# Optimization experiments

Measured on AMD Instinct MI355X. Metric: run time of the kernel, lower is better.

Reference implementation:

```python
import jax, jax.numpy as jnp
import numpy as np

B, S, D, E, K = 8, 4096, 2048, 64, 8


def setup_inputs() -> dict:
    key = jax.random.key(0)
    ks = jax.random.split(key, 4)
    x = jax.random.normal(ks[0], (B, S, D), dtype=jnp.float32)
    noise = jax.random.normal(ks[1], (B, S, E), dtype=jnp.float32)
    scale = 1.0 / np.sqrt(D)
    W_linear = jax.random.normal(ks[2], (E, D), dtype=jnp.float32) * scale
    W_noise = jax.random.normal(ks[3], (E, D), dtype=jnp.float32) * scale
    b_linear = jnp.zeros((E,), dtype=jnp.float32)
    b_noise = jnp.zeros((E,), dtype=jnp.float32)
    return {"x": x, "noise": noise, "W_linear": W_linear, "b_linear": b_linear,
            "W_noise": W_noise, "b_noise": b_noise}


def reference(x, noise, W_linear, b_linear, W_noise, b_noise):
    # logits / noise_logits: [B,S,E]
    logits = jnp.einsum('bsd,ed->bse', x, W_linear) + b_linear
    noise_logits = jnp.einsum('bsd,ed->bse', x, W_noise) + b_noise
    noisy = logits + noise * jax.nn.softplus(noise_logits)
    topk_vals, indices = jax.lax.top_k(noisy, K)  # [B,S,K]
    # scatter top-k values into a -inf tensor, softmax over experts
    flat_vals = topk_vals.reshape(-1, K)
    flat_idx = indices.reshape(-1, K)
    N = flat_idx.shape[0]
    sparse = jnp.full((N, E), -jnp.inf, dtype=noisy.dtype)
    sparse = sparse.at[jnp.arange(N)[:, None], flat_idx].set(flat_vals)
    router_output = jax.nn.softmax(sparse, axis=-1).reshape(B, S, E)
    return router_output, indices
```

## Files before the change

### kernel.cpp

```cpp
#include <hip/hip_runtime.h>
#include <hip/hip_bf16.h>
#include <math.h>

namespace {
constexpr int DD = 2048;
constexpr int EE = 64;
constexpr int KK = 8;
constexpr int TPB = 64;
constexpr int MS = 128;
constexpr int NMEGA = DD / MS;
constexpr int NTH = 256;
constexpr int XB = TPB * MS * 4;
constexpr float TAU = 2e-4f;
}

typedef __attribute__((ext_vector_type(8))) short short8;
typedef __attribute__((ext_vector_type(4))) float f32x4;

#define RES(t, e) res[(t) * 129 + (e)]

__device__ inline void split_bf16(float v, ushort& h, ushort& l) {
    __hip_bfloat16 hb = __float2bfloat16(v);
    float hf = __bfloat162float(hb);
    __hip_bfloat16 lb = __float2bfloat16(v - hf);
    h = __builtin_bit_cast(ushort, hb);
    l = __builtin_bit_cast(ushort, lb);
}

__device__ inline void conv_tile(const float4& A, const float4& B, short8& hi, short8& lo) {
    const float f[8] = {A.x, A.y, A.z, A.w, B.x, B.y, B.z, B.w};
#pragma unroll
    for (int i = 0; i < 8; ++i) {
        ushort h, l;
        split_bf16(f[i], h, l);
        hi[i] = (short)h;
        lo[i] = (short)l;
    }
}

__device__ inline void gload_lds16(const void* g, void* l) {
    __builtin_amdgcn_global_load_lds(
        (const __attribute__((address_space(1))) unsigned int*)g,
        (__attribute__((address_space(3))) unsigned int*)l,
        16, 0, 0);
}

#define STAGE(m_, c_)                                                                  \
    do {                                                                               \
        unsigned char* xb_ = smem + (c_) * XB;                                         \
        _Pragma("unroll")                                                              \
        for (int j = 0; j < 8; ++j) {                                                  \
            const int row_ = (w * 8 + j) * 2 + (lane >> 5);                            \
            const int u_   = lane & 31;                                                \
            const float* g_ = x + (tok0 + row_) * (long)DD + (long)(m_) * MS           \
                              + ((u_ ^ (row_ & 7)) << 2);                              \
            gload_lds16(g_, xb_ + (w * 8 + j) * 1024);                                 \
        }                                                                              \
    } while (0)

#define LOADW(dst_, m_, ss_)                                                           \
    do {                                                                               \
        _Pragma("unroll")                                                              \
        for (int el_ = 0; el_ < 4; ++el_) {                                            \
            const size_t b_ = ((size_t)(((m_) * 4 + (ss_)) * 8 + eq * 4 + el_)) * 128; \
            dst_[el_ * 2]     = wp[b_];                                                \
            dst_[el_ * 2 + 1] = wp[b_ + 64];                                           \
        }                                                                              \
    } while (0)

__global__ __launch_bounds__(256)
void prep_w(const float* __restrict__ Wl, const float* __restrict__ Wn,
            ushort* __restrict__ wsB)
{
    const int t    = blockIdx.x * 256 + threadIdx.x;
    const int lane = t & 63;
    const int et   = (t >> 6) & 7;
    const int s    = t >> 9;
    const int e    = et * 16 + (lane & 15);
    const int k    = s * 32 + ((lane >> 4) * 8);
    const float* src = (e < EE) ? &Wl[(long)e * DD + k] : &Wn[(long)(e - EE) * DD + k];
    const float4 f0 = *reinterpret_cast<const float4*>(src);
    const float4 f1 = *reinterpret_cast<const float4*>(src + 4);
    const float f[8] = {f0.x, f0.y, f0.z, f0.w, f1.x, f1.y, f1.z, f1.w};
    uint hw[4], lw[4];
#pragma unroll
    for (int j = 0; j < 4; ++j) {
        ushort h0, l0, h1, l1;
        split_bf16(f[2 * j], h0, l0);
        split_bf16(f[2 * j + 1], h1, l1);
        hw[j] = (uint)h0 | ((uint)h1 << 16);
        lw[j] = (uint)l0 | ((uint)l1 << 16);
    }
    const size_t chunk = ((size_t)(s * 8 + et)) * 1024;
    *reinterpret_cast<uint4*>(&wsB[chunk + lane * 8])       = make_uint4(hw[0], hw[1], hw[2], hw[3]);
    *reinterpret_cast<uint4*>(&wsB[chunk + 512 + lane * 8]) = make_uint4(lw[0], lw[1], lw[2], lw[3]);
}

__global__ __launch_bounds__(NTH, 2)
void router_main(const float* __restrict__ x,
                 const float* __restrict__ noise,
                 const ushort* __restrict__ wsB,
                 const float* __restrict__ Wl, const float* __restrict__ bl,
                 const float* __restrict__ Wn, const float* __restrict__ bn,
                 float* __restrict__ out_router, float* __restrict__ out_idx)
{
    __shared__ __align__(16) unsigned char smem[2 * XB];
    __shared__ float  tkv[TPB][KK];
    __shared__ int    tki[TPB][KK];
    __shared__ int    cand[TPB][10];
    __shared__ int    amb_list[TPB];
    __shared__ int    amb_count;
    __shared__ double dsh[20];

    const int tid  = threadIdx.x;
    const int lane = tid & 63;
    const int w    = tid >> 6;
    const int mh   = w >> 1;
    const int eq   = w & 1;
    const long tok0 = (long)blockIdx.x * TPB;
    if (tid == 0) amb_count = 0;

    const uint4* wp = reinterpret_cast<const uint4*>(wsB) + lane;

    f32x4 acc[2][4];
#pragma unroll
    for (int mt = 0; mt < 2; ++mt)
#pragma unroll
        for (int e = 0; e < 4; ++e) acc[mt][e] = {0.f, 0.f, 0.f, 0.f};

    uint4 W0[8], W1[8], W2[8], W3[8];
    STAGE(0, 0);
    LOADW(W0, 0, 0);
    LOADW(W1, 0, 1);
    __syncthreads();

    const int colr = lane & 15;
    const int krow = lane >> 4;

    for (int m = 0; m < NMEGA; ++m) {
        const int cur = m & 1;
        if (m + 1 < NMEGA) STAGE(m + 1, cur ^ 1);
        const unsigned char* xb = smem + cur * XB;
#pragma unroll
        for (int ss = 0; ss < 4; ++ss) {
            if (ss == 0)      LOADW(W2, m, 2);
            else if (ss == 1) LOADW(W3, m, 3);
            else if (ss == 2) { if (m + 1 < NMEGA) LOADW(W0, m + 1, 0); }
            else              { if (m + 1 < NMEGA) LOADW(W1, m + 1, 1); }

            short8 ah[2], al[2];
#pragma unroll
            for (int mt = 0; mt < 2; ++mt) {
                const int r = mh * 32 + mt * 16 + colr;
                const unsigned char* base = xb + r * 512;
                const int v0 = ss * 8 + krow * 2;
                const float4 f0 = *reinterpret_cast<const float4*>(base + ((v0 ^ (r & 7)) << 4));
                const float4 f1 = *reinterpret_cast<const float4*>(base + (((v0 + 1) ^ (r & 7)) << 4));
                conv_tile(f0, f1, ah[mt], al[mt]);
            }
            const uint4* Wc = (ss == 0) ? W0 : (ss == 1) ? W1 : (ss == 2) ? W2 : W3;
#pragma unroll
            for (int el = 0; el < 4; ++el) {
                const short8 bh  = __builtin_bit_cast(short8, Wc[el * 2]);
                const short8 bl2 = __builtin_bit_cast(short8, Wc[el * 2 + 1]);
                acc[0][el] = __builtin_amdgcn_mfma_f32_16x16x32_bf16(ah[0], bh,  acc[0][el], 0, 0, 0);
                acc[1][el] = __builtin_amdgcn_mfma_f32_16x16x32_bf16(ah[1], bh,  acc[1][el], 0, 0, 0);
                acc[0][el] = __builtin_amdgcn_mfma_f32_16x16x32_bf16(al[0], bh,  acc[0][el], 0, 0, 0);
                acc[1][el] = __builtin_amdgcn_mfma_f32_16x16x32_bf16(al[1], bh,  acc[1][el], 0, 0, 0);
                acc[0][el] = __builtin_amdgcn_mfma_f32_16x16x32_bf16(ah[0], bl2, acc[0][el], 0, 0, 0);
                acc[1][el] = __builtin_amdgcn_mfma_f32_16x16x32_bf16(ah[1], bl2, acc[1][el], 0, 0, 0);
            }
        }
        __syncthreads();
    }

    float* res = reinterpret_cast<float*>(smem);
    {
        const int rg = (lane >> 4) * 4;
#pragma unroll
        for (int mt = 0; mt < 2; ++mt)
#pragma unroll
            for (int el = 0; el < 4; ++el) {
                const int e = (eq * 4 + el) * 16 + colr;
                const float bias = (e < EE) ? bl[e] : bn[e - EE];
#pragma unroll
                for (int r = 0; r < 4; ++r)
                    RES(mh * 32 + mt * 16 + rg + r, e) = acc[mt][el][r] + bias;
            }
    }
    __syncthreads();

    {
        const int t  = tid >> 2;
        const int e0 = (tid & 3) * 16;
        const float* nrow = &noise[(tok0 + t) * (long)EE];
#pragma unroll 4
        for (int j = 0; j < 16; ++j) {
            const int e = e0 + j;
            const float z  = RES(t, EE + e);
            const float sp = fmaxf(z, 0.f) + log1pf(expf(-fabsf(z)));
            RES(t, e) = RES(t, e) + nrow[e] * sp;
        }
    }
    __syncthreads();

    {
        const int t   = tid >> 2;
        const int sub = tid & 3;
        float lv[10]; int li[10];
#pragma unroll
        for (int k = 0; k < 10; ++k) {
            float best = -INFINITY;
            int bi = sub * 16;
#pragma unroll
            for (int j = 0; j < 16; ++j) {
                const int e = sub * 16 + j;
                const float v = RES(t, e);
                if (v > best) { best = v; bi = e; }
            }
#pragma unroll
            for (int m = 1; m < 4; m <<= 1) {
                const float ov = __shfl_xor(best, m, 64);
                const int   oi = __shfl_xor(bi, m, 64);
                if (ov > best || (ov == best && oi < bi)) { best = ov; bi = oi; }
            }
            lv[k] = best; li[k] = bi;
            if ((bi >> 4) == sub) RES(t, bi) = -INFINITY;
        }
        bool amb = false;
#pragma unroll
        for (int k = 0; k < 9; ++k) amb |= (lv[k] - lv[k + 1] < TAU);
        const float mmax = lv[0];
        float p[KK];
        float sm = 0.f;
#pragma unroll
        for (int k = 0; k < KK; ++k) { p[k] = expf(lv[k] - mmax); sm += p[k]; }
        const float inv = 1.f / sm;
        if (sub == 0) {
#pragma unroll
            for (int k = 0; k < KK; ++k) { tkv[t][k] = p[k] * inv; tki[t][k] = li[k]; }
            if (amb) {
                const int pos = atomicAdd(&amb_count, 1);
                amb_list[pos] = t;
#pragma unroll
                for (int c = 0; c < 10; ++c) cand[t][c] = li[c];
            }
        }
    }
    __syncthreads();

    const int namb = amb_count;
    for (int a = 0; a < namb; ++a) {
        const int t = amb_list[a];
        {
            const float4* xsrc = reinterpret_cast<const float4*>(&x[(tok0 + t) * (long)DD]);
            float4* xd = reinterpret_cast<float4*>(smem);
            xd[tid * 2]     = xsrc[tid * 2];
            xd[tid * 2 + 1] = xsrc[tid * 2 + 1];
        }
        __syncthreads();
        {
            const int g  = tid >> 3;
            const int gs = tid & 7;
            double dsum = 0.0;
            if (g < 20) {
                const int c = (g < 10) ? g : g - 10;
                const int e = cand[t][c];
                const float* wr = (g < 10) ? &Wl[(long)e * DD] : &Wn[(long)e * DD];
                const float* xs = reinterpret_cast<const float*>(smem);
                for (int k = gs * 4; k < DD; k += 32) {
                    const float4 xv = *reinterpret_cast<const float4*>(&xs[k]);
                    const float4 wv = *reinterpret_cast<const float4*>(&wr[k]);
                    dsum = fma((double)xv.x, (double)wv.x, dsum);
                    dsum = fma((double)xv.y, (double)wv.y, dsum);
                    dsum = fma((double)xv.z, (double)wv.z, dsum);
                    dsum = fma((double)xv.w, (double)wv.w, dsum);
                }
            }
#pragma unroll
            for (int m = 1; m < 8; m <<= 1) dsum += __shfl_xor(dsum, m, 64);
            if (g < 20 && (tid & 7) == 0) dsh[g] = dsum;
        }
        __syncthreads();
        if (tid < 64) {
            double val; int idx;
            if (tid < 10) {
                const int e = cand[t][tid];
                const double v  = dsh[tid] + (double)bl[e];
                const double z  = dsh[10 + tid] + (double)bn[e];
                const double sp = fmax(z, 0.0) + log1p(exp(-fabs(z)));
                val = v + (double)noise[(tok0 + t) * (long)EE + e] * sp;
                idx = e;
            } else { val = -INFINITY; idx = 64 + tid; }
            double sel[KK]; int sidx[KK];
#pragma unroll
            for (int k = 0; k < KK; ++k) {
                double mv = val; int mi = idx;
#pragma unroll
                for (int m = 1; m < 64; m <<= 1) {
                    const double ov = __shfl_xor(mv, m, 64);
                    const int   oi = __shfl_xor(mi, m, 64);
                    if (ov > mv || (ov == mv && oi < mi)) { mv = ov; mi = oi; }
                }
                sel[k] = mv; sidx[k] = mi;
                if (idx == mi) val = -INFINITY;
            }
            if (tid == 0) {
                const double mx = sel[0];
                double p[KK]; double sm = 0.0;
#pragma unroll
                for (int k = 0; k < KK; ++k) { p[k] = exp(sel[k] - mx); sm += p[k]; }
                const double inv = 1.0 / sm;
#pragma unroll
                for (int k = 0; k < KK; ++k) {
                    tkv[t][k] = (float)(p[k] * inv);
                    tki[t][k] = sidx[k];
                }
            }
        }
        __syncthreads();
    }

    {
        const int t  = tid >> 2;
        const int e0 = (tid & 3) * 16;
        int   ki[KK];
        float kv[KK];
#pragma unroll
        for (int k = 0; k < KK; ++k) { ki[k] = tki[t][k]; kv[k] = tkv[t][k]; }
        float4 v[4];
        float* vf = reinterpret_cast<float*>(v);
#pragma unroll
        for (int j = 0; j < 16; ++j) {
            float val = 0.f;
#pragma unroll
            for (int k = 0; k < KK; ++k)
                val = (ki[k] == e0 + j) ? kv[k] : val;
            vf[j] = val;
        }
        float4* dst = reinterpret_cast<float4*>(&out_router[(tok0 + t) * (long)EE + e0]);
#pragma unroll
        for (int q = 0; q < 4; ++q) dst[q] = v[q];
    }
    {
        const int f = tid * 2;
        const int t = f >> 3;
        const int k0i = f & 7;
        out_idx[(tok0 + t) * (long)KK + k0i]     = (float)tki[t][k0i];
        out_idx[(tok0 + t) * (long)KK + k0i + 1] = (float)tki[t][k0i + 1];
    }
}

extern "C" void kernel_launch(void* const* d_in, const int* in_sizes, int n_in,
                              void* d_out, int out_size, void* d_ws, size_t ws_size,
                              hipStream_t stream) {
    const float* x     = (const float*)d_in[0];
    const float* noise = (const float*)d_in[1];
    const float* Wl    = (const float*)d_in[2];
    const float* bl    = (const float*)d_in[3];
    const float* Wn    = (const float*)d_in[4];
    const float* bn    = (const float*)d_in[5];

    const int M = in_sizes[0] / DD;
    float* out_router = (float*)d_out;
    float* out_idx    = (float*)d_out + (long)M * EE;
    ushort* wsB = (ushort*)d_ws;

    hipLaunchKernelGGL(prep_w, dim3(128), dim3(256), 0, stream, Wl, Wn, wsB);
    hipLaunchKernelGGL(router_main, dim3(M / TPB), dim3(NTH), 0, stream,
                       x, noise, wsB, Wl, bl, Wn, bn, out_router, out_idx);
}
```

Before: 160.6 us.

## Double block to 512 threads, each wave computing one 16-token tile

The main router kernel now uses 8 waves per block instead of 4. Each wave handles a single 16-row M tile instead of two, which halves the accumulator and A-fragment registers, and launch bounds now request 4 blocks per CU. The staging, softplus/noise, and output-write phases are redistributed over 512 threads, and the top-k and ambiguity phases are gated to the first 256 threads. This raises parallelism and latency hiding but loses the reuse of each loaded B (weight) fragment across two M tiles, so per-wave weight register traffic doubles relative to MFMA work.

```diff
diff --git a/kernel.cpp b/kernel.cpp
--- a/kernel.cpp
+++ b/kernel.cpp
@@ -9,7 +9,7 @@
 constexpr int TPB = 64;
 constexpr int MS = 128;
 constexpr int NMEGA = DD / MS;
-constexpr int NTH = 256;
+constexpr int NTH = 512;
 constexpr int XB = TPB * MS * 4;
 constexpr float TAU = 2e-4f;
 }
@@ -49,12 +49,13 @@
     do {                                                                               \
         unsigned char* xb_ = smem + (c_) * XB;                                         \
         _Pragma("unroll")                                                              \
-        for (int j = 0; j < 8; ++j) {                                                  \
-            const int row_ = (w * 8 + j) * 2 + (lane >> 5);                            \
+        for (int j = 0; j < 4; ++j) {                                                  \
+            const int ch_  = w * 4 + j;                                                \
+            const int row_ = ch_ * 2 + (lane >> 5);                                    \
             const int u_   = lane & 31;                                                \
             const float* g_ = x + (tok0 + row_) * (long)DD + (long)(m_) * MS           \
                               + ((u_ ^ (row_ & 7)) << 2);                              \
-            gload_lds16(g_, xb_ + (w * 8 + j) * 1024);                                 \
+            gload_lds16(g_, xb_ + ch_ * 1024);                                         \
         }                                                                              \
     } while (0)
 
@@ -96,7 +97,7 @@
     *reinterpret_cast<uint4*>(&wsB[chunk + 512 + lane * 8]) = make_uint4(lw[0], lw[1], lw[2], lw[3]);
 }
 
-__global__ __launch_bounds__(NTH, 2)
+__global__ __launch_bounds__(NTH, 4)
 void router_main(const float* __restrict__ x,
                  const float* __restrict__ noise,
                  const ushort* __restrict__ wsB,
@@ -115,18 +116,16 @@
     const int tid  = threadIdx.x;
     const int lane = tid & 63;
     const int w    = tid >> 6;
-    const int mh   = w >> 1;
+    const int tg   = w >> 1;
     const int eq   = w & 1;
     const long tok0 = (long)blockIdx.x * TPB;
     if (tid == 0) amb_count = 0;
 
     const uint4* wp = reinterpret_cast<const uint4*>(wsB) + lane;
 
-    f32x4 acc[2][4];
-#pragma unroll
-    for (int mt = 0; mt < 2; ++mt)
-#pragma unroll
-        for (int e = 0; e < 4; ++e) acc[mt][e] = {0.f, 0.f, 0.f, 0.f};
+    f32x4 acc[4];
+#pragma unroll
+    for (int e = 0; e < 4; ++e) acc[e] = {0.f, 0.f, 0.f, 0.f};
 
     uint4 W0[8], W1[8], W2[8], W3[8];
     STAGE(0, 0);
@@ -148,27 +147,23 @@
             else if (ss == 2) { if (m + 1 < NMEGA) LOADW(W0, m + 1, 0); }
             else              { if (m + 1 < NMEGA) LOADW(W1, m + 1, 1); }
 
-            short8 ah[2], al[2];
-#pragma unroll
-            for (int mt = 0; mt < 2; ++mt) {
-                const int r = mh * 32 + mt * 16 + colr;
+            short8 ah, al;
+            {
+                const int r = tg * 16 + colr;
                 const unsigned char* base = xb + r * 512;
                 const int v0 = ss * 8 + krow * 2;
                 const float4 f0 = *reinterpret_cast<const float4*>(base + ((v0 ^ (r & 7)) << 4));
                 const float4 f1 = *reinterpret_cast<const float4*>(base + (((v0 + 1) ^ (r & 7)) << 4));
-                conv_tile(f0, f1, ah[mt], al[mt]);
+                conv_tile(f0, f1, ah, al);
             }
             const uint4* Wc = (ss == 0) ? W0 : (ss == 1) ? W1 : (ss == 2) ? W2 : W3;
 #pragma unroll
             for (int el = 0; el < 4; ++el) {
                 const short8 bh  = __builtin_bit_cast(short8, Wc[el * 2]);
                 const short8 bl2 = __builtin_bit_cast(short8, Wc[el * 2 + 1]);
-                acc[0][el] = __builtin_amdgcn_mfma_f32_16x16x32_bf16(ah[0], bh,  acc[0][el], 0, 0, 0);
-                acc[1][el] = __builtin_amdgcn_mfma_f32_16x16x32_bf16(ah[1], bh,  acc[1][el], 0, 0, 0);
-                acc[0][el] = __builtin_amdgcn_mfma_f32_16x16x32_bf16(al[0], bh,  acc[0][el], 0, 0, 0);
-                acc[1][el] = __builtin_amdgcn_mfma_f32_16x16x32_bf16(al[1], bh,  acc[1][el], 0, 0, 0);
-                acc[0][el] = __builtin_amdgcn_mfma_f32_16x16x32_bf16(ah[0], bl2, acc[0][el], 0, 0, 0);
-                acc[1][el] = __builtin_amdgcn_mfma_f32_16x16x32_bf16(ah[1], bl2, acc[1][el], 0, 0, 0);
+                acc[el] = __builtin_amdgcn_mfma_f32_16x16x32_bf16(ah, bh,  acc[el], 0, 0, 0);
+                acc[el] = __builtin_amdgcn_mfma_f32_16x16x32_bf16(al, bh,  acc[el], 0, 0, 0);
+                acc[el] = __builtin_amdgcn_mfma_f32_16x16x32_bf16(ah, bl2, acc[el], 0, 0, 0);
             }
         }
         __syncthreads();
@@ -178,33 +173,33 @@
     {
         const int rg = (lane >> 4) * 4;
 #pragma unroll
-        for (int mt = 0; mt < 2; ++mt)
-#pragma unroll
-            for (int el = 0; el < 4; ++el) {
-                const int e = (eq * 4 + el) * 16 + colr;
-                const float bias = (e < EE) ? bl[e] : bn[e - EE];
-#pragma unroll
-                for (int r = 0; r < 4; ++r)
-                    RES(mh * 32 + mt * 16 + rg + r, e) = acc[mt][el][r] + bias;
-            }
+        for (int el = 0; el < 4; ++el) {
+            const int e = (eq * 4 + el) * 16 + colr;
+            const float bias = (e < EE) ? bl[e] : bn[e - EE];
+#pragma unroll
+            for (int r = 0; r < 4; ++r)
+                RES(tg * 16 + rg + r, e) = acc[el][r] + bias;
+        }
     }
     __syncthreads();
 
     {
-        const int t  = tid >> 2;
-        const int e0 = (tid & 3) * 16;
-        const float* nrow = &noise[(tok0 + t) * (long)EE];
-#pragma unroll 4
-        for (int j = 0; j < 16; ++j) {
+        const int t  = tid >> 3;
+        const int e0 = (tid & 7) * 8;
+        const float4 n0 = *reinterpret_cast<const float4*>(&noise[(tok0 + t) * (long)EE + e0]);
+        const float4 n1 = *reinterpret_cast<const float4*>(&noise[(tok0 + t) * (long)EE + e0 + 4]);
+        const float nv[8] = {n0.x, n0.y, n0.z, n0.w, n1.x, n1.y, n1.z, n1.w};
+#pragma unroll
+        for (int j = 0; j < 8; ++j) {
             const int e = e0 + j;
             const float z  = RES(t, EE + e);
             const float sp = fmaxf(z, 0.f) + log1pf(expf(-fabsf(z)));
-            RES(t, e) = RES(t, e) + nrow[e] * sp;
+            RES(t, e) = RES(t, e) + nv[j] * sp;
         }
     }
     __syncthreads();
 
-    {
+    if (tid < 256) {
         const int t   = tid >> 2;
         const int sub = tid & 3;
         float lv[10]; int li[10];
@@ -252,7 +247,7 @@
     const int namb = amb_count;
     for (int a = 0; a < namb; ++a) {
         const int t = amb_list[a];
-        {
+        if (tid < 256) {
             const float4* xsrc = reinterpret_cast<const float4*>(&x[(tok0 + t) * (long)DD]);
             float4* xd = reinterpret_cast<float4*>(smem);
             xd[tid * 2]     = xsrc[tid * 2];
@@ -322,32 +317,29 @@
     }
 
     {
-        const int t  = tid >> 2;
-        const int e0 = (tid & 3) * 16;
+        const int t  = tid >> 3;
+        const int e0 = (tid & 7) * 8;
         int   ki[KK];
         float kv[KK];
 #pragma unroll
         for (int k = 0; k < KK; ++k) { ki[k] = tki[t][k]; kv[k] = tkv[t][k]; }
-        float4 v[4];
-        float* vf = reinterpret_cast<float*>(v);
-#pragma unroll
-        for (int j = 0; j < 16; ++j) {
+        float v[8];
+#pragma unroll
+        for (int j = 0; j < 8; ++j) {
             float val = 0.f;
 #pragma unroll
             for (int k = 0; k < KK; ++k)
                 val = (ki[k] == e0 + j) ? kv[k] : val;
-            vf[j] = val;
-        }
-        float4* dst = reinterpret_cast<float4*>(&out_router[(tok0 + t) * (long)EE + e0]);
-#pragma unroll
-        for (int q = 0; q < 4; ++q) dst[q] = v[q];
+            v[j] = val;
+        }
+        float* dst = &out_router[(tok0 + t) * (long)EE + e0];
+        *reinterpret_cast<float4*>(dst)     = make_float4(v[0], v[1], v[2], v[3]);
+        *reinterpret_cast<float4*>(dst + 4) = make_float4(v[4], v[5], v[6], v[7]);
     }
     {
-        const int f = tid * 2;
-        const int t = f >> 3;
-        const int k0i = f & 7;
-        out_idx[(tok0 + t) * (long)KK + k0i]     = (float)tki[t][k0i];
-        out_idx[(tok0 + t) * (long)KK + k0i + 1] = (float)tki[t][k0i + 1];
+        const int t = tid >> 3;
+        const int k = tid & 7;
+        out_idx[(tok0 + t) * (long)KK + k] = (float)tki[t][k];
     }
 }
 
```

New measurement: 185.0 us. 1.15x slower.

## Halve x mega-tile and W register buffers to run four blocks per CU

Applied to the files above, without the earlier changes.

Shrinks the per-stage x tile from 128 to 64 columns, which halves the LDS double buffer, and restructures the W register prefetch into two current plus two next sets. Launch bounds now ask for 4 blocks per CU instead of 2. The aim is more waves per CU to hide global-load latency in this memory-bound GEMV-like router. The cost is twice as many loop iterations and barriers per block, plus a risk of spills under the tighter register budget. The shared buffer is fixed at 33024 bytes, presumably so the later reuse of smem as the result array (64x129 floats) still fits.

```diff
diff --git a/kernel.cpp b/kernel.cpp
--- a/kernel.cpp
+++ b/kernel.cpp
@@ -7,7 +7,7 @@
 constexpr int EE = 64;
 constexpr int KK = 8;
 constexpr int TPB = 64;
-constexpr int MS = 128;
+constexpr int MS = 64;
 constexpr int NMEGA = DD / MS;
 constexpr int NTH = 256;
 constexpr int XB = TPB * MS * 4;
@@ -49,12 +49,13 @@
     do {                                                                               \
         unsigned char* xb_ = smem + (c_) * XB;                                         \
         _Pragma("unroll")                                                              \
-        for (int j = 0; j < 8; ++j) {                                                  \
-            const int row_ = (w * 8 + j) * 2 + (lane >> 5);                            \
-            const int u_   = lane & 31;                                                \
+        for (int j = 0; j < 4; ++j) {                                                  \
+            const int ch_  = w * 4 + j;                                                \
+            const int row_ = ch_ * 4 + (lane >> 4);                                    \
+            const int u_   = lane & 15;                                                \
             const float* g_ = x + (tok0 + row_) * (long)DD + (long)(m_) * MS           \
                               + ((u_ ^ (row_ & 7)) << 2);                              \
-            gload_lds16(g_, xb_ + (w * 8 + j) * 1024);                                 \
+            gload_lds16(g_, xb_ + ch_ * 1024);                                         \
         }                                                                              \
     } while (0)
 
@@ -62,9 +63,36 @@
     do {                                                                               \
         _Pragma("unroll")                                                              \
         for (int el_ = 0; el_ < 4; ++el_) {                                            \
-            const size_t b_ = ((size_t)(((m_) * 4 + (ss_)) * 8 + eq * 4 + el_)) * 128; \
+            const size_t b_ = ((size_t)(((m_) * 2 + (ss_)) * 8 + eq * 4 + el_)) * 128; \
             dst_[el_ * 2]     = wp[b_];                                                \
             dst_[el_ * 2 + 1] = wp[b_ + 64];                                           \
+        }                                                                              \
+    } while (0)
+
+#define SUBSTEP(Wc_, ss_)                                                              \
+    do {                                                                               \
+        short8 ah[2], al[2];                                                           \
+        _Pragma("unroll")                                                              \
+        for (int mt = 0; mt < 2; ++mt) {                                               \
+            const int r = mh * 32 + mt * 16 + colr;                                    \
+            const unsigned char* base = xb + r * 256;                                  \
+            const int v0 = (ss_) * 8 + krow * 2;                                       \
+            const float4 f0 = *reinterpret_cast<const float4*>(                        \
+                base + ((v0 ^ (r & 7)) << 4));                                         \
+            const float4 f1 = *reinterpret_cast<const float4*>(                        \
+                base + (((v0 + 1) ^ (r & 7)) << 4));                                   \
+            conv_tile(f0, f1, ah[mt], al[mt]);                                         \
+        }                                                                              \
+        _Pragma("unroll")                                                              \
+        for (int el = 0; el < 4; ++el) {                                               \
+            const short8 bh  = __builtin_bit_cast(short8, Wc_[el * 2]);                \
+            const short8 bl2 = __builtin_bit_cast(short8, Wc_[el * 2 + 1]);            \
+            acc[0][el] = __builtin_amdgcn_mfma_f32_16x16x32_bf16(ah[0], bh,  acc[0][el], 0, 0, 0); \
+            acc[1][el] = __builtin_amdgcn_mfma_f32_16x16x32_bf16(ah[1], bh,  acc[1][el], 0, 0, 0); \
+            acc[0][el] = __builtin_amdgcn_mfma_f32_16x16x32_bf16(al[0], bh,  acc[0][el], 0, 0, 0); \
+            acc[1][el] = __builtin_amdgcn_mfma_f32_16x16x32_bf16(al[1], bh,  acc[1][el], 0, 0, 0); \
+            acc[0][el] = __builtin_amdgcn_mfma_f32_16x16x32_bf16(ah[0], bl2, acc[0][el], 0, 0, 0); \
+            acc[1][el] = __builtin_amdgcn_mfma_f32_16x16x32_bf16(ah[1], bl2, acc[1][el], 0, 0, 0); \
         }                                                                              \
     } while (0)
 
@@ -96,7 +124,7 @@
     *reinterpret_cast<uint4*>(&wsB[chunk + 512 + lane * 8]) = make_uint4(lw[0], lw[1], lw[2], lw[3]);
 }
 
-__global__ __launch_bounds__(NTH, 2)
+__global__ __launch_bounds__(NTH, 4)
 void router_main(const float* __restrict__ x,
                  const float* __restrict__ noise,
                  const ushort* __restrict__ wsB,
@@ -104,7 +132,7 @@
                  const float* __restrict__ Wn, const float* __restrict__ bn,
                  float* __restrict__ out_router, float* __restrict__ out_idx)
 {
-    __shared__ __align__(16) unsigned char smem[2 * XB];
+    __shared__ __align__(16) unsigned char smem[33024];
     __shared__ float  tkv[TPB][KK];
     __shared__ int    tki[TPB][KK];
     __shared__ int    cand[TPB][10];
@@ -128,10 +156,10 @@
 #pragma unroll
         for (int e = 0; e < 4; ++e) acc[mt][e] = {0.f, 0.f, 0.f, 0.f};
 
-    uint4 W0[8], W1[8], W2[8], W3[8];
+    uint4 Wa[8], Wb[8], Na[8], Nb[8];
     STAGE(0, 0);
-    LOADW(W0, 0, 0);
-    LOADW(W1, 0, 1);
+    LOADW(Wa, 0, 0);
+    LOADW(Wb, 0, 1);
     __syncthreads();
 
     const int colr = lane & 15;
@@ -141,36 +169,14 @@
         const int cur = m & 1;
         if (m + 1 < NMEGA) STAGE(m + 1, cur ^ 1);
         const unsigned char* xb = smem + cur * XB;
-#pragma unroll
-        for (int ss = 0; ss < 4; ++ss) {
-            if (ss == 0)      LOADW(W2, m, 2);
-            else if (ss == 1) LOADW(W3, m, 3);
-            else if (ss == 2) { if (m + 1 < NMEGA) LOADW(W0, m + 1, 0); }
-            else              { if (m + 1 < NMEGA) LOADW(W1, m + 1, 1); }
-
-            short8 ah[2], al[2];
-#pragma unroll
-            for (int mt = 0; mt < 2; ++mt) {
-                const int r = mh * 32 + mt * 16 + colr;
-                const unsigned char* base = xb + r * 512;
-                const int v0 = ss * 8 + krow * 2;
-                const float4 f0 = *reinterpret_cast<const float4*>(base + ((v0 ^ (r & 7)) << 4));
-                const float4 f1 = *reinterpret_cast<const float4*>(base + (((v0 + 1) ^ (r & 7)) << 4));
-                conv_tile(f0, f1, ah[mt], al[mt]);
-            }
-            const uint4* Wc = (ss == 0) ? W0 : (ss == 1) ? W1 : (ss == 2) ? W2 : W3;
-#pragma unroll
-            for (int el = 0; el < 4; ++el) {
-                const short8 bh  = __builtin_bit_cast(short8, Wc[el * 2]);
-                const short8 bl2 = __builtin_bit_cast(short8, Wc[el * 2 + 1]);
-                acc[0][el] = __builtin_amdgcn_mfma_f32_16x16x32_bf16(ah[0], bh,  acc[0][el], 0, 0, 0);
-                acc[1][el] = __builtin_amdgcn_mfma_f32_16x16x32_bf16(ah[1], bh,  acc[1][el], 0, 0, 0);
-                acc[0][el] = __builtin_amdgcn_mfma_f32_16x16x32_bf16(al[0], bh,  acc[0][el], 0, 0, 0);
-                acc[1][el] = __builtin_amdgcn_mfma_f32_16x16x32_bf16(al[1], bh,  acc[1][el], 0, 0, 0);
-                acc[0][el] = __builtin_amdgcn_mfma_f32_16x16x32_bf16(ah[0], bl2, acc[0][el], 0, 0, 0);
-                acc[1][el] = __builtin_amdgcn_mfma_f32_16x16x32_bf16(ah[1], bl2, acc[1][el], 0, 0, 0);
-            }
-        }
+
+        if (m + 1 < NMEGA) LOADW(Na, m + 1, 0);
+        SUBSTEP(Wa, 0);
+        if (m + 1 < NMEGA) LOADW(Nb, m + 1, 1);
+        SUBSTEP(Wb, 1);
+
+#pragma unroll
+        for (int q = 0; q < 8; ++q) { Wa[q] = Na[q]; Wb[q] = Nb[q]; }
         __syncthreads();
     }
 
```

Measured after the change: 211.7 us. +31.8%, slower.
